# Kernel optimization log

Measured on AMD Instinct MI355X. Metric: run time of the kernel, lower is better.

The kernel has to match this reference:

```python
import jax, jax.numpy as jnp
import numpy as np

B, C, I = 4096, 256, 16          # nodes, channels (num_features), per-channel irrep dim (lmax=3)
K3, K2, K1 = 23, 4, 1            # num symmetric-contraction paths per correlation order


def setup_inputs() -> dict:
    key = jax.random.key(0)
    ks = jax.random.split(key, 8)
    return {
        "node_feats": jax.random.normal(ks[0], (B, C, I), jnp.float32),
        "U3": jax.random.normal(ks[1], (I, I, I, K3), jnp.float32),  # fixed CG basis, corr=3
        "U2": jax.random.normal(ks[2], (I, I, K2), jnp.float32),     # fixed CG basis, corr=2
        "U1": jax.random.normal(ks[3], (I, K1), jnp.float32),        # fixed CG basis, corr=1
        "w3": jax.random.normal(ks[4], (C, K3), jnp.float32),        # per-channel weights, corr=3
        "w2": jax.random.normal(ks[5], (C, K2), jnp.float32),
        "w1": jax.random.normal(ks[6], (C, K1), jnp.float32),
        "W_lin": jax.random.normal(ks[7], (C, C), jnp.float32),      # o3.Linear (scalars) weight
    }


def reference(node_feats, U3, U2, U1, w3, w2, w1, W_lin):
    """MACE symmetric contraction (ProductBasisBlock), vectorized over channels.

    Per-channel math (correlation = 3):
      out = einsum('pqik,k,bi->bpq', U3, w3[c], x[:,c])          # main
      c2  = einsum('pqk,k->pq', U2, w2[c]); out = einsum('bpi,bi->bp', c2+out, x[:,c])
      c1  = einsum('pk,k->p',  U1, w1[c]); out = einsum('bi,bi->b',  c1+out, x[:,c])
    The Python-level per-channel loop is replaced by a channel axis c in the einsums.
    """
    x = node_feats                                            # (B, C, I)
    # --- main contraction at correlation order 3 ---
    U3w = jnp.einsum('pqik,ck->cpqi', U3, w3)                 # (C, I, I, I)
    out = jnp.einsum('cpqi,bci->bcpq', U3w, x)                # (B, C, I, I)
    # --- corr = 2 ---
    c2 = jnp.einsum('pik,ck->cpi', U2, w2)                    # (C, I, I)
    out = jnp.einsum('bcpi,bci->bcp', c2[None] + out, x)      # (B, C, I)
    # --- corr = 1 ---
    c1 = jnp.einsum('ik,ck->ci', U1, w1)                      # (C, I)
    out = jnp.einsum('bci,bci->bc', c1[None] + out, x)        # (B, C)
    # --- o3.Linear on the scalar (0e) outputs: x @ W with 1/sqrt(fan_in) path norm ---
    inv_sqrt_fan_in = 1.0 / np.sqrt(C).astype(np.float32)
    return jnp.einsum('bc,cd->bd', out, W_lin) * inv_sqrt_fan_in
```

## Files before the change

kernel.cpp:

```cpp
#include <hip/hip_runtime.h>


#define B_NODES 4096
#define C_CH    256
#define K3      23
#define K2      4

#define KSTEPS   9
#define KB_ELEMS (KSTEPS * 64 * 8)
#define KB_U32   (KB_ELEMS / 2)

#define TILES_PER_WAVE 8

typedef short    short8 __attribute__((ext_vector_type(8)));
typedef float    f32x4  __attribute__((ext_vector_type(4)));
typedef unsigned u32x4  __attribute__((ext_vector_type(4)));

static constexpr size_t OFF_BF_BYTES = 0;
static constexpr size_t OFF_ST_BYTES = (size_t)C_CH * KB_ELEMS * 2;

__device__ inline unsigned short f2bf_rne(float f) {
  unsigned u = __builtin_bit_cast(unsigned, f);
  unsigned r = u + 0x7FFFu + ((u >> 16) & 1u);
  return (unsigned short)(r >> 16);
}

#define F2U(f) __builtin_bit_cast(unsigned, (f))
#define PK2(YH, YL) __builtin_amdgcn_perm(F2U(YH), F2U(YL), 0x07060302u)

__global__ __launch_bounds__(256) void precompute_bfrag(
    const float* __restrict__ U3, const float* __restrict__ U2,
    const float* __restrict__ U1, const float* __restrict__ w3,
    const float* __restrict__ w2, const float* __restrict__ w1,
    unsigned int* __restrict__ bfrag_u32) {
  const int c = blockIdx.x;
  const int t = threadIdx.x;

  __shared__ float su3w[4096];
  for (int l = t; l < 4096; l += 256) {
    float a = 0.f;
#pragma unroll
    for (int k3 = 0; k3 < K3; ++k3)
      a += U3[(size_t)l * K3 + k3] * w3[c * K3 + k3];
    su3w[l] = a;
  }
  __syncthreads();

  const int lane = t >> 2;
  const int jj   = (t & 3) * 2;
  const int p = lane & 15, g = lane >> 4;

#pragma unroll
  for (int s = 0; s < 8; ++s) {
    const int q = 2 * s + (g >> 1);
    float v0 = 0.f, v1 = 0.f;
#pragma unroll
    for (int e = 0; e < 2; ++e) {
      const int i = (g & 1) * 8 + jj + e;
      float a = 0.f;
      if (q < i)
        a = su3w[(p * 16 + q) * 16 + i] + su3w[(p * 16 + i) * 16 + q];
      else if (q == i)
        a = su3w[(p * 16 + q) * 16 + q];
      if (e == 0) v0 = a; else v1 = a;
    }
    bfrag_u32[(size_t)c * KB_U32 + s * 256 + t] =
        (unsigned)f2bf_rne(v0) | ((unsigned)f2bf_rne(v1) << 16);
  }

  {
    float v0 = 0.f, v1 = 0.f;
#pragma unroll
    for (int e = 0; e < 2; ++e) {
      const int k = 256 + g * 8 + jj + e;
      float a = 0.f;
      if (k < 272) {
        const int q = k - 256;
#pragma unroll
        for (int k2 = 0; k2 < K2; ++k2)
          a += U2[(size_t)(p * 16 + q) * K2 + k2] * w2[c * K2 + k2];
      } else if (k == 272) {
        a = U1[p] * w1[c];
      }
      if (e == 0) v0 = a; else v1 = a;
    }
    bfrag_u32[(size_t)c * KB_U32 + 8 * 256 + t] =
        (unsigned)f2bf_rne(v0) | ((unsigned)f2bf_rne(v1) << 16);
  }
}


#define QSTEP(BF, XQ, ACC)                                                     \
  __builtin_amdgcn_mfma_f32_16x16x32_bf16((BF),                                \
      __builtin_bit_cast(short8, (u32x4){                                      \
          PK2((XQ) * xh1, (XQ) * xh0), PK2((XQ) * xh3, (XQ) * xh2),            \
          PK2((XQ) * xh5, (XQ) * xh4), PK2((XQ) * xh7, (XQ) * xh6)}),          \
      (ACC), 0, 0, 0)

#define TILE_BODY(X0, X1, X2, X3, Tc)                                          \
  do {                                                                         \
    const float xh0 = ghi ? (X2).x : (X0).x;                                   \
    const float xh1 = ghi ? (X2).y : (X0).y;                                   \
    const float xh2 = ghi ? (X2).z : (X0).z;                                   \
    const float xh3 = ghi ? (X2).w : (X0).w;                                   \
    const float xh4 = ghi ? (X3).x : (X1).x;                                   \
    const float xh5 = ghi ? (X3).y : (X1).y;                                   \
    const float xh6 = ghi ? (X3).z : (X1).z;                                   \
    const float xh7 = ghi ? (X3).w : (X1).w;                                   \
    const float xq0 = gq ? (X0).y : (X0).x;                                    \
    const float xq1 = gq ? (X0).w : (X0).z;                                    \
    const float xq2 = gq ? (X1).y : (X1).x;                                    \
    const float xq3 = gq ? (X1).w : (X1).z;                                    \
    const float xq4 = gq ? (X2).y : (X2).x;                                    \
    const float xq5 = gq ? (X2).w : (X2).z;                                    \
    const float xq6 = gq ? (X3).y : (X3).x;                                    \
    const float xq7 = gq ? (X3).w : (X3).z;                                    \
    f32x4 acc  = (f32x4){0.f, 0.f, 0.f, 0.f};                                  \
    f32x4 acc2 = (f32x4){0.f, 0.f, 0.f, 0.f};                                  \
    acc  = QSTEP(bf0, xq0, acc);                                               \
    acc2 = QSTEP(bf1, xq1, acc2);                                              \
    acc  = QSTEP(bf2, xq2, acc);                                               \
    acc2 = QSTEP(bf3, xq3, acc2);                                              \
    acc  = QSTEP(bf4, xq4, acc);                                               \
    acc2 = QSTEP(bf5, xq5, acc2);                                              \
    acc  = QSTEP(bf6, xq6, acc);                                               \
    acc2 = QSTEP(bf7, xq7, acc2);                                              \
    {                                                                          \
      const float y0 = glin ? xh0 : cst;                                       \
      const float y1 = glin ? xh1 : 0.f;                                       \
      const float y2 = glin ? xh2 : 0.f;                                       \
      const float y3 = glin ? xh3 : 0.f;                                       \
      const float y4 = glin ? xh4 : 0.f;                                       \
      const float y5 = glin ? xh5 : 0.f;                                       \
      const float y6 = glin ? xh6 : 0.f;                                       \
      const float y7 = glin ? xh7 : 0.f;                                       \
      acc = __builtin_amdgcn_mfma_f32_16x16x32_bf16(bf8,                       \
          __builtin_bit_cast(short8, (u32x4){PK2(y1, y0), PK2(y3, y2),         \
                                             PK2(y5, y4), PK2(y7, y6)}),       \
          acc, 0, 0, 0);                                                       \
    }                                                                          \
    acc = acc + acc2;                                                          \
    const float4 xs = (g & 2) ? ((g & 1) ? (X3) : (X2))                        \
                              : ((g & 1) ? (X1) : (X0));                       \
    float v = acc[0] * xs.x + acc[1] * xs.y + acc[2] * xs.z + acc[3] * xs.w;   \
    v += __shfl_xor(v, 16);                                                    \
    v += __shfl_xor(v, 32);                                                    \
    if (g == 0) sTrow[(Tc) * 16 + n] = v;                                      \
  } while (0)

__global__ __launch_bounds__(256)
__attribute__((amdgpu_waves_per_eu(2, 4)))
void contract_mfma(
    const float* __restrict__ x, const short8* __restrict__ bfragv,
    float* __restrict__ sT) {
  const int c0  = blockIdx.x * 4;
  const int nb0 = blockIdx.y * (TILES_PER_WAVE * 16);
  const int t   = threadIdx.x;
  const int w = t >> 6, lane = t & 63, n = lane & 15, g = lane >> 4;
  const int ch = c0 + w;

  const short8* bp = bfragv + (size_t)ch * (KSTEPS * 64);
  const short8 bf0 = bp[0 * 64 + lane];
  const short8 bf1 = bp[1 * 64 + lane];
  const short8 bf2 = bp[2 * 64 + lane];
  const short8 bf3 = bp[3 * 64 + lane];
  const short8 bf4 = bp[4 * 64 + lane];
  const short8 bf5 = bp[5 * 64 + lane];
  const short8 bf6 = bp[6 * 64 + lane];
  const short8 bf7 = bp[7 * 64 + lane];
  const short8 bf8 = bp[8 * 64 + lane];

  const bool  ghi  = (g & 1) != 0;
  const bool  gq   = ((g >> 1) & 1) != 0;
  const bool  glin = (g < 2);
  const float cst  = (g == 2) ? 1.0f : 0.0f;
  float* sTrow = sT + (size_t)ch * B_NODES + nb0;

  const float* xb = x + (size_t)(nb0 + n) * (C_CH * 16) + (size_t)ch * 16;
  const size_t tstride = (size_t)16 * C_CH * 16;

  float4 a0, a1, a2, a3, b0, b1, b2, b3;
  {
    const float4* p = (const float4*)xb;
    a0 = p[0]; a1 = p[1]; a2 = p[2]; a3 = p[3];
  }

#pragma unroll
  for (int TT = 0; TT < TILES_PER_WAVE / 2; ++TT) {
    {
      const float4* p = (const float4*)(xb + (size_t)(2 * TT + 1) * tstride);
      b0 = p[0]; b1 = p[1]; b2 = p[2]; b3 = p[3];
    }
    TILE_BODY(a0, a1, a2, a3, 2 * TT);
    if (TT + 1 < TILES_PER_WAVE / 2) {
      const float4* p = (const float4*)(xb + (size_t)(2 * TT + 2) * tstride);
      a0 = p[0]; a1 = p[1]; a2 = p[2]; a3 = p[3];
    }
    TILE_BODY(b0, b1, b2, b3, 2 * TT + 1);
  }
}

__global__ __launch_bounds__(256) void linear_kernel(
    const float* __restrict__ sT, const float* __restrict__ W,
    float* __restrict__ out) {
  const int b0 = blockIdx.x * 64;
  const int d0 = blockIdx.y * 64;
  const int t  = threadIdx.x;
  const int tx = t & 15;
  const int ty = t >> 4;

  __shared__ float As[16][64];
  __shared__ float Bs[16][64];
  float acc[4][4] = {};

  for (int k0 = 0; k0 < C_CH; k0 += 16) {
    const int kk  = t >> 6;
    const int col = t & 63;
#pragma unroll
    for (int r = 0; r < 4; ++r) {
      As[kk + r * 4][col] = sT[(size_t)(k0 + kk + r * 4) * B_NODES + b0 + col];
      Bs[kk + r * 4][col] = W[(size_t)(k0 + kk + r * 4) * C_CH + d0 + col];
    }
    __syncthreads();
#pragma unroll
    for (int k = 0; k < 16; ++k) {
      float a[4], bv[4];
#pragma unroll
      for (int i = 0; i < 4; ++i) a[i] = As[k][ty * 4 + i];
#pragma unroll
      for (int j = 0; j < 4; ++j) bv[j] = Bs[k][tx * 4 + j];
#pragma unroll
      for (int i = 0; i < 4; ++i)
#pragma unroll
        for (int j = 0; j < 4; ++j) acc[i][j] += a[i] * bv[j];
    }
    __syncthreads();
  }

#pragma unroll
  for (int i = 0; i < 4; ++i) {
    float4 v = make_float4(acc[i][0] * 0.0625f, acc[i][1] * 0.0625f,
                           acc[i][2] * 0.0625f, acc[i][3] * 0.0625f);
    *(float4*)(out + (size_t)(b0 + ty * 4 + i) * C_CH + d0 + tx * 4) = v;
  }
}

extern "C" void kernel_launch(void* const* d_in, const int* in_sizes, int n_in,
                              void* d_out, int out_size, void* d_ws, size_t ws_size,
                              hipStream_t stream) {
  const float* x  = (const float*)d_in[0];
  const float* U3 = (const float*)d_in[1];
  const float* U2 = (const float*)d_in[2];
  const float* U1 = (const float*)d_in[3];
  const float* w3 = (const float*)d_in[4];
  const float* w2 = (const float*)d_in[5];
  const float* w1 = (const float*)d_in[6];
  const float* Wl = (const float*)d_in[7];

  unsigned int* bfrag = (unsigned int*)((char*)d_ws + OFF_BF_BYTES);
  float*        sT    = (float*)((char*)d_ws + OFF_ST_BYTES);
  float*        out   = (float*)d_out;

  precompute_bfrag<<<dim3(C_CH), dim3(256), 0, stream>>>(
      U3, U2, U1, w3, w2, w1, bfrag);
  contract_mfma<<<dim3(C_CH / 4, B_NODES / (TILES_PER_WAVE * 16)), dim3(256), 0, stream>>>(
      x, (const short8*)bfrag, sT);
  linear_kernel<<<dim3(B_NODES / 64, C_CH / 64), dim3(256), 0, stream>>>(sT, Wl, out);
}
```

Measured before the change: 153.2 us.

## Repack upper-triangular K-steps to drop zero blocks from MFMA chain

Reorganizes the symmetric (q,i) packing of the third-order tensor so the lower-right 8x8 block, which is only half populated, is covered by two K-steps instead of four. The main contraction therefore issues seven MFMAs per tile instead of nine and keeps fewer B fragments resident in registers. In exchange the x-operand selection for the new steps needs a four-way select per lane group, and the prep kernel layout has to match the new fragment order exactly.

```diff
diff --git a/kernel.cpp b/kernel.cpp
--- a/kernel.cpp
+++ b/kernel.cpp
@@ -6,7 +6,7 @@
 #define K3      23
 #define K2      4
 
-#define KSTEPS   9
+#define KSTEPS   7
 #define KB_ELEMS (KSTEPS * 64 * 8)
 #define KB_U32   (KB_ELEMS / 2)
 
@@ -51,7 +51,7 @@
   const int p = lane & 15, g = lane >> 4;
 
 #pragma unroll
-  for (int s = 0; s < 8; ++s) {
+  for (int s = 0; s < 4; ++s) {
     const int q = 2 * s + (g >> 1);
     float v0 = 0.f, v1 = 0.f;
 #pragma unroll
@@ -68,6 +68,24 @@
         (unsigned)f2bf_rne(v0) | ((unsigned)f2bf_rne(v1) << 16);
   }
 
+#pragma unroll
+  for (int s = 4; s < 6; ++s) {
+    const int q = 8 + (s - 4) * 4 + g;
+    float v0 = 0.f, v1 = 0.f;
+#pragma unroll
+    for (int e = 0; e < 2; ++e) {
+      const int i = 8 + jj + e;
+      float a = 0.f;
+      if (q < i)
+        a = su3w[(p * 16 + q) * 16 + i] + su3w[(p * 16 + i) * 16 + q];
+      else if (q == i)
+        a = su3w[(p * 16 + q) * 16 + q];
+      if (e == 0) v0 = a; else v1 = a;
+    }
+    bfrag_u32[(size_t)c * KB_U32 + s * 256 + t] =
+        (unsigned)f2bf_rne(v0) | ((unsigned)f2bf_rne(v1) << 16);
+  }
+
   {
     float v0 = 0.f, v1 = 0.f;
 #pragma unroll
@@ -84,17 +102,17 @@
       }
       if (e == 0) v0 = a; else v1 = a;
     }
-    bfrag_u32[(size_t)c * KB_U32 + 8 * 256 + t] =
+    bfrag_u32[(size_t)c * KB_U32 + 6 * 256 + t] =
         (unsigned)f2bf_rne(v0) | ((unsigned)f2bf_rne(v1) << 16);
   }
 }
 
 
-#define QSTEP(BF, XQ, ACC)                                                     \
+#define QSTEP8(BF, XQ, H0, H1, H2, H3, H4, H5, H6, H7, ACC)                    \
   __builtin_amdgcn_mfma_f32_16x16x32_bf16((BF),                                \
       __builtin_bit_cast(short8, (u32x4){                                      \
-          PK2((XQ) * xh1, (XQ) * xh0), PK2((XQ) * xh3, (XQ) * xh2),            \
-          PK2((XQ) * xh5, (XQ) * xh4), PK2((XQ) * xh7, (XQ) * xh6)}),          \
+          PK2((XQ) * (H1), (XQ) * (H0)), PK2((XQ) * (H3), (XQ) * (H2)),        \
+          PK2((XQ) * (H5), (XQ) * (H4)), PK2((XQ) * (H7), (XQ) * (H6))}),      \
       (ACC), 0, 0, 0)
 
 #define TILE_BODY(X0, X1, X2, X3, Tc)                                          \
@@ -111,20 +129,22 @@
     const float xq1 = gq ? (X0).w : (X0).z;                                    \
     const float xq2 = gq ? (X1).y : (X1).x;                                    \
     const float xq3 = gq ? (X1).w : (X1).z;                                    \
-    const float xq4 = gq ? (X2).y : (X2).x;                                    \
-    const float xq5 = gq ? (X2).w : (X2).z;                                    \
-    const float xq6 = gq ? (X3).y : (X3).x;                                    \
-    const float xq7 = gq ? (X3).w : (X3).z;                                    \
+    const float xq4 = (g == 0) ? (X2).x                                        \
+                   : (g == 1) ? (X2).y                                         \
+                   : (g == 2) ? (X2).z : (X2).w;                  \
+    const float xq5 = (g == 0) ? (X3).x                                        \
+                   : (g == 1) ? (X3).y                                         \
+                   : (g == 2) ? (X3).z : (X3).w;                  \
     f32x4 acc  = (f32x4){0.f, 0.f, 0.f, 0.f};                                  \
     f32x4 acc2 = (f32x4){0.f, 0.f, 0.f, 0.f};                                  \
-    acc  = QSTEP(bf0, xq0, acc);                                               \
-    acc2 = QSTEP(bf1, xq1, acc2);                                              \
-    acc  = QSTEP(bf2, xq2, acc);                                               \
-    acc2 = QSTEP(bf3, xq3, acc2);                                              \
-    acc  = QSTEP(bf4, xq4, acc);                                               \
-    acc2 = QSTEP(bf5, xq5, acc2);                                              \
-    acc  = QSTEP(bf6, xq6, acc);                                               \
-    acc2 = QSTEP(bf7, xq7, acc2);                                              \
+    acc  = QSTEP8(bf0, xq0, xh0, xh1, xh2, xh3, xh4, xh5, xh6, xh7, acc);      \
+    acc2 = QSTEP8(bf1, xq1, xh0, xh1, xh2, xh3, xh4, xh5, xh6, xh7, acc2);     \
+    acc  = QSTEP8(bf2, xq2, xh0, xh1, xh2, xh3, xh4, xh5, xh6, xh7, acc);      \
+    acc2 = QSTEP8(bf3, xq3, xh0, xh1, xh2, xh3, xh4, xh5, xh6, xh7, acc2);     \
+    acc  = QSTEP8(bf4, xq4, (X2).x, (X2).y, (X2).z, (X2).w,                    \
+                  (X3).x, (X3).y, (X3).z, (X3).w, acc);                        \
+    acc2 = QSTEP8(bf5, xq5, (X2).x, (X2).y, (X2).z, (X2).w,                    \
+                  (X3).x, (X3).y, (X3).z, (X3).w, acc2);                       \
     {                                                                          \
       const float y0 = glin ? xh0 : cst;                                       \
       const float y1 = glin ? xh1 : 0.f;                                       \
@@ -134,7 +154,7 @@
       const float y5 = glin ? xh5 : 0.f;                                       \
       const float y6 = glin ? xh6 : 0.f;                                       \
       const float y7 = glin ? xh7 : 0.f;                                       \
-      acc = __builtin_amdgcn_mfma_f32_16x16x32_bf16(bf8,                       \
+      acc = __builtin_amdgcn_mfma_f32_16x16x32_bf16(bf6,                       \
           __builtin_bit_cast(short8, (u32x4){PK2(y1, y0), PK2(y3, y2),         \
                                              PK2(y5, y4), PK2(y7, y6)}),       \
           acc, 0, 0, 0);                                                       \
@@ -167,8 +187,6 @@
   const short8 bf4 = bp[4 * 64 + lane];
   const short8 bf5 = bp[5 * 64 + lane];
   const short8 bf6 = bp[6 * 64 + lane];
-  const short8 bf7 = bp[7 * 64 + lane];
-  const short8 bf8 = bp[8 * 64 + lane];
 
   const bool  ghi  = (g & 1) != 0;
   const bool  gq   = ((g >> 1) & 1) != 0;
```

New measurement: 151.3 us. Within noise of the previous version (-1.2%).
